# Kernel optimization log

Hardware: AMD Instinct MI355X
Metric: run time of the kernel (lower is better)

Reference implementation:

```python
import jax, jax.numpy as jnp
import numpy as np

EPS = 1e-5

def bn_eval(x, p):
    # p: [4, C] = gamma, beta, running_mean, running_var; channel-last broadcast
    g, b, m, v = p[0], p[1], p[2], p[3]
    return (x - m) * (g / jnp.sqrt(v + EPS)) + b

def _bn_params(k, c):
    k1, k2, k3, k4 = jax.random.split(k, 4)
    gamma = jax.random.uniform(k1, (c,)) + 0.5
    beta = jax.random.normal(k2, (c,)) * 0.1
    mean = jax.random.normal(k3, (c,)) * 0.1
    var = jax.random.uniform(k4, (c,)) + 0.5
    return jnp.stack([gamma, beta, mean, var])

def _lin(k, fan_in, fan_out):
    bound = 1.0 / np.sqrt(fan_in)
    kw, kb = jax.random.split(k)
    w = jax.random.uniform(kw, (fan_in, fan_out), minval=-bound, maxval=bound)
    b = jax.random.uniform(kb, (fan_out,), minval=-bound, maxval=bound)
    return w, b

def setup_inputs() -> dict:
    key = jax.random.key(0)
    B, N, S, C, G = 2, 4096, 16, 256, 8
    ks = jax.random.split(key, 20)
    feats = jax.random.normal(ks[0], (B, N, C), dtype=jnp.float32)
    coords = jax.random.normal(ks[1], (B, N, 3), dtype=jnp.float32)
    index = jax.random.randint(ks[2], (B, N, S), 0, N, dtype=jnp.int32)
    wq, bq = _lin(ks[3], C, C); bnq = _bn_params(ks[4], C)
    wk, bk = _lin(ks[5], C, C); bnk = _bn_params(ks[6], C)
    wv, bv = _lin(ks[7], C, C)
    pm_w1, pm_b1 = _lin(ks[8], 3, C); pm_bn = _bn_params(ks[9], C)
    pm_w2, pm_b2 = _lin(ks[10], C, C)
    pb_w1, pb_b1 = _lin(ks[11], 3, C); pb_bn = _bn_params(ks[12], C)
    pb_w2, pb_b2 = _lin(ks[13], C, C)
    we_w1, we_b1 = _lin(ks[14], C, G); we_bn = _bn_params(ks[15], G)
    we_w2, we_b2 = _lin(ks[16], G, G)
    return dict(feats=feats, coords=coords, index=index,
                wq=wq, bq=bq, bnq=bnq, wk=wk, bk=bk, bnk=bnk, wv=wv, bv=bv,
                pm_w1=pm_w1, pm_b1=pm_b1, pm_bn=pm_bn, pm_w2=pm_w2, pm_b2=pm_b2,
                pb_w1=pb_w1, pb_b1=pb_b1, pb_bn=pb_bn, pb_w2=pb_w2, pb_b2=pb_b2,
                we_w1=we_w1, we_b1=we_b1, we_bn=we_bn, we_w2=we_w2, we_b2=we_b2)

def reference(feats, coords, index,
              wq, bq, bnq, wk, bk, bnk, wv, bv,
              pm_w1, pm_b1, pm_bn, pm_w2, pm_b2,
              pb_w1, pb_b1, pb_bn, pb_w2, pb_b2,
              we_w1, we_b1, we_bn, we_w2, we_b2):
    B, N, C = feats.shape
    S = index.shape[2]
    G = we_w1.shape[1]
    q = jax.nn.relu(bn_eval(feats @ wq + bq, bnq))                       # [B,N,C]
    k = jax.nn.relu(bn_eval(feats @ wk + bk, bnk))                       # [B,N,C]
    v = feats @ wv + bv                                                   # [B,N,C]
    idx = index.reshape(B, N * S)
    key_g = jnp.take_along_axis(k, idx[:, :, None], axis=1).reshape(B, N, S, C)
    val_g = jnp.take_along_axis(v, idx[:, :, None], axis=1).reshape(B, N, S, C)
    crd_g = jnp.take_along_axis(coords, idx[:, :, None], axis=1).reshape(B, N, S, 3)
    relation_qk = key_g - q[:, :, None, :]                                # [B,N,S,C]
    pos = coords[:, :, None, :] - crd_g                                   # [B,N,S,3]
    pem = jax.nn.relu(bn_eval(pos @ pm_w1 + pm_b1, pm_bn)) @ pm_w2 + pm_b2
    relation_qk = relation_qk * pem
    peb = jax.nn.relu(bn_eval(pos @ pb_w1 + pb_b1, pb_bn)) @ pb_w2 + pb_b2
    relation_qk = relation_qk + peb
    val_g = val_g + peb
    w = jax.nn.relu(bn_eval(relation_qk @ we_w1 + we_b1, we_bn)) @ we_w2 + we_b2  # [B,N,S,G]
    w = jax.nn.softmax(w, axis=2)                                         # softmax over neighbors
    val_g = val_g.reshape(B, N, S, G, C // G)
    out = jnp.einsum('bnsgi,bnsg->bngi', val_g, w).reshape(B, N, C)
    return out
```

## Files before the change

kernel.cpp:

```cpp
#include <hip/hip_runtime.h>
#include <hip/hip_bf16.h>


typedef __attribute__((ext_vector_type(8))) short bf16x8_t;
typedef __attribute__((ext_vector_type(4))) float f32x4_t;

#define BN_EPS 1e-5f
#define WSYNC() asm volatile("s_waitcnt lgkmcnt(0)" ::: "memory")

__device__ __forceinline__ float blo(unsigned int v) {
    union { unsigned int u; float f; } x; x.u = v << 16; return x.f;
}
__device__ __forceinline__ float bhi(unsigned int v) {
    union { unsigned int u; float f; } x; x.u = v & 0xffff0000u; return x.f;
}
__device__ __forceinline__ unsigned int fbits(float f) {
    union { float f; unsigned int u; } x; x.f = f; return x.u;
}
__device__ __forceinline__ unsigned short f2b(float f) {
    unsigned int u = fbits(f);
    return (unsigned short)((u + 0x7fffu + ((u >> 16) & 1u)) >> 16);
}
__device__ __forceinline__ float b2f(unsigned short h) {
    union { unsigned int u; float f; } x; x.u = ((unsigned int)h) << 16; return x.f;
}
__device__ __forceinline__ unsigned int f2bpk(float a, float b) {
    union { __hip_bfloat162 h; unsigned int u; } x;
    x.h = __float22bfloat162_rn(make_float2(a, b));
    return x.u;
}
__device__ __forceinline__ unsigned int relpair(unsigned int kb, unsigned int qb,
                                                unsigned int pm_, unsigned int pb_) {
    float r0 = (blo(kb) - blo(qb)) * blo(pm_) + blo(pb_);
    float r1 = (bhi(kb) - bhi(qb)) * bhi(pm_) + bhi(pb_);
    return f2bpk(r0, r1);
}

__global__ __launch_bounds__(256) void k_prep(
    const float* __restrict__ wq, const float* __restrict__ wk,
    const float* __restrict__ wv, const float* __restrict__ pm2,
    const float* __restrict__ pb2,
    const float* __restrict__ pm_w1, const float* __restrict__ pm_b1,
    const float* __restrict__ pm_bn,
    const float* __restrict__ pb_w1, const float* __restrict__ pb_b1,
    const float* __restrict__ pb_bn,
    const float* __restrict__ we_w1,
    const float* __restrict__ bq, const float* __restrict__ bnq,
    const float* __restrict__ bk, const float* __restrict__ bnk,
    const float* __restrict__ bv,
    unsigned short* __restrict__ wsT, unsigned short* __restrict__ w1F,
    unsigned short* __restrict__ we1TF, float* __restrict__ SS)
{
    const int bid = blockIdx.x, t = threadIdx.x;
    if (bid < 160) {
        __shared__ unsigned short T[32][72];
        const int mat = bid >> 5;
        const int kk  = (bid >> 2) & 7;
        const int ntq = bid & 3;
        const float* s = (mat == 0) ? wq : (mat == 1) ? wk : (mat == 2) ? wv
                         : (mat == 3) ? pm2 : pb2;
        {
            int c = t & 63, r0 = t >> 6;
            for (int i = 0; i < 8; ++i) {
                int r = r0 + i * 4;
                T[r][c] = f2b(s[(kk * 32 + r) * 256 + ntq * 64 + c]);
            }
        }
        __syncthreads();
        {
            int seg = t >> 6, lane = t & 63;
            int col = seg * 16 + (lane & 15);
            int kr  = (lane >> 4) * 8;
            unsigned int v[8];
            #pragma unroll
            for (int j = 0; j < 8; ++j) v[j] = T[kr + j][col];
            uint4 o;
            o.x = v[0] | (v[1] << 16);
            o.y = v[2] | (v[3] << 16);
            o.z = v[4] | (v[5] << 16);
            o.w = v[6] | (v[7] << 16);
            *(uint4*)(wsT + mat * 65536 + (ntq * 4 + seg) * 4096 + kk * 512 + lane * 8) = o;
        }
    } else if (bid == 160) {
        int c = t;
        int nt = c >> 4, l15 = c & 15;
        float sm = pm_bn[c] / sqrtf(pm_bn[768 + c] + BN_EPS);
        float sb = pb_bn[c] / sqrtf(pb_bn[768 + c] + BN_EPS);
        float W[2][4];
        W[0][0] = pm_w1[c] * sm; W[0][1] = pm_w1[256 + c] * sm;
        W[0][2] = pm_w1[512 + c] * sm;
        W[0][3] = (pm_b1[c] - pm_bn[512 + c]) * sm + pm_bn[256 + c];
        W[1][0] = pb_w1[c] * sb; W[1][1] = pb_w1[256 + c] * sb;
        W[1][2] = pb_w1[512 + c] * sb;
        W[1][3] = (pb_b1[c] - pb_bn[512 + c]) * sb + pb_bn[256 + c];
        for (int pass = 0; pass < 2; ++pass) {
            unsigned short xh = f2b(W[pass][0]), xl = f2b(W[pass][0] - b2f(xh));
            unsigned short yh = f2b(W[pass][1]), yl = f2b(W[pass][1] - b2f(yh));
            unsigned short zh = f2b(W[pass][2]), zl = f2b(W[pass][2] - b2f(zh));
            unsigned short bh = f2b(W[pass][3]), bl = f2b(W[pass][3] - b2f(bh));
            unsigned short sl[16] = { xh, xh, xl, yh, yh, yl, zh, zh, zl,
                                      bh, bl, 0, 0, 0, 0, 0 };
            for (int q = 0; q < 4; ++q)
                for (int j = 0; j < 8; ++j)
                    w1F[((pass * 16 + nt) * 64 + q * 16 + l15) * 8 + j] =
                        (q < 2) ? sl[q * 8 + j] : (unsigned short)0;
        }
    } else {
        for (int j = 0; j < 8; ++j) {
            int e = t * 8 + j;
            int g = e >> 8, c = e & 255;
            we1TF[g * 256 + c] = f2b(we_w1[c * 8 + g]);
        }
        int c = t;
        float sq = bnq[c] / sqrtf(bnq[768 + c] + BN_EPS);
        SS[c]        = sq;
        SS[256 + c]  = (bq[c] - bnq[512 + c]) * sq + bnq[256 + c];
        float sk = bnk[c] / sqrtf(bnk[768 + c] + BN_EPS);
        SS[512 + c]  = sk;
        SS[768 + c]  = (bk[c] - bnk[512 + c]) * sk + bnk[256 + c];
        SS[1024 + c] = 1.0f;
        SS[1280 + c] = bv[c];
    }
}

__global__ __launch_bounds__(256) void k_qkv(
    const float* __restrict__ feats,
    const unsigned short* __restrict__ wT,
    const float* __restrict__ SS,
    unsigned short* __restrict__ qkv)
{
    __shared__ unsigned short A[32][264];
    const int t    = threadIdx.x;
    const int widx = blockIdx.x >> 8;
    const int mb   = blockIdx.x & 255;

    for (int i = 0; i < 8; ++i) {
        int row = 4 * i + (t >> 6), col = (t & 63) * 4;
        float4 f = *(const float4*)(feats + (mb * 32 + row) * 256 + col);
        *(uint2*)&A[row][col] = make_uint2(f2bpk(f.x, f.y), f2bpk(f.z, f.w));
    }
    __syncthreads();

    const int lane = t & 63, w = t >> 6;
    const int ln15 = lane & 15, quad = lane >> 4;
    const int mt = w & 1, nh = w >> 1;

    bf16x8_t afr[8];
    #pragma unroll
    for (int kk = 0; kk < 8; ++kk)
        afr[kk] = *(const bf16x8_t*)&A[mt * 16 + ln15][kk * 32 + quad * 8];

    const unsigned short* W = wT + widx * 65536;
    unsigned short* dst = qkv + (size_t)widx * 8192 * 256;

    f32x4_t acc[8];
    for (int j = 0; j < 8; ++j) acc[j] = (f32x4_t){0.f, 0.f, 0.f, 0.f};

    #pragma unroll
    for (int kk = 0; kk < 8; ++kk) {
        #pragma unroll
        for (int j = 0; j < 8; ++j) {
            int nt = nh * 8 + j;
            bf16x8_t wfr = *(const bf16x8_t*)(W + ((nt * 8 + kk) * 64 + lane) * 8);
            acc[j] = __builtin_amdgcn_mfma_f32_16x16x32_bf16(wfr, afr[kk], acc[j], 0, 0, 0);
        }
    }

    const float* S = SS + widx * 512;
    const int row = mb * 32 + mt * 16 + ln15;
    #pragma unroll
    for (int j = 0; j < 8; ++j) {
        int n0 = (nh * 8 + j) * 16 + quad * 4;
        float4 s4 = *(const float4*)(S + n0);
        float4 h4 = *(const float4*)(S + 256 + n0);
        float y0 = acc[j][0] * s4.x + h4.x;
        float y1 = acc[j][1] * s4.y + h4.y;
        float y2 = acc[j][2] * s4.z + h4.z;
        float y3 = acc[j][3] * s4.w + h4.w;
        if (widx < 2) {
            y0 = fmaxf(y0, 0.f); y1 = fmaxf(y1, 0.f);
            y2 = fmaxf(y2, 0.f); y3 = fmaxf(y3, 0.f);
        }
        *(uint2*)(dst + (size_t)row * 256 + n0) =
            make_uint2(f2bpk(y0, y1), f2bpk(y2, y3));
    }
}

__global__ __launch_bounds__(512, 4) void k_main(
    const float* __restrict__ coords,
    const int*   __restrict__ index,
    const unsigned short* __restrict__ qm,
    const unsigned short* __restrict__ km,
    const unsigned short* __restrict__ vm,
    const unsigned short* __restrict__ pmw2F,
    const unsigned short* __restrict__ pbw2F,
    const unsigned short* __restrict__ w1F,
    const unsigned short* __restrict__ we1TF,
    const float* __restrict__ pm_b2, const float* __restrict__ pb_b2,
    const float* __restrict__ we_b1, const float* __restrict__ we_bn,
    const float* __restrict__ we_w2, const float* __restrict__ we_b2,
    float* __restrict__ out)
{
    __shared__ unsigned short bufR[64][264];
    __shared__ unsigned short bufP[64][264];
    __shared__ unsigned short posX[64][32];
    __shared__ float us_[8][16][10];
    __shared__ float we2s[8][8];
    __shared__ float web2[8], swe8[8], dwe8[8];

    const int t   = threadIdx.x;
    const int P0  = blockIdx.x * 4;
    const int bb_ = P0 >> 12;
    const int w = t >> 6, lane = t & 63;
    const int ln15 = lane & 15, quad = lane >> 4;
    const int p   = w >> 1, sub = w & 1;
    const int R0  = p * 16;
    const int Pg  = P0 + p;

    const int rg = (bb_ << 12) + index[Pg * 16 + ln15];

    if (t < 64) {
        int m  = t;
        int Pr = P0 + (m >> 4);
        int rs = (bb_ << 12) + index[Pr * 16 + (m & 15)];
        float x = coords[Pr * 3 + 0] - coords[rs * 3 + 0];
        float y = coords[Pr * 3 + 1] - coords[rs * 3 + 1];
        float z = coords[Pr * 3 + 2] - coords[rs * 3 + 2];
        unsigned short xh = f2b(x), xl = f2b(x - b2f(xh));
        unsigned short yh = f2b(y), yl = f2b(y - b2f(yh));
        unsigned short zh = f2b(z), zl = f2b(z - b2f(zh));
        const unsigned short one = 0x3f80;
        posX[m][0] = xh; posX[m][1] = xl; posX[m][2] = xh;
        posX[m][3] = yh; posX[m][4] = yl; posX[m][5] = yh;
        posX[m][6] = zh; posX[m][7] = zl; posX[m][8] = zh;
        posX[m][9] = one; posX[m][10] = one;
        #pragma unroll
        for (int j2 = 11; j2 < 32; ++j2) posX[m][j2] = 0;
        we2s[m >> 3][m & 7] = we_w2[m];
    }
    if (t < 8) {
        float s = we_bn[t] / sqrtf(we_bn[24 + t] + BN_EPS);
        swe8[t] = s;
        dwe8[t] = (we_b1[t] - we_bn[16 + t]) * s + we_bn[8 + t];
        web2[t] = we_b2[t];
    }
    __syncthreads();

    bf16x8_t afrP[4];
    #pragma unroll
    for (int mt = 0; mt < 4; ++mt)
        afrP[mt] = *(const bf16x8_t*)&posX[mt * 16 + ln15][quad * 8];

    {
        f32x4_t hb[2][4];
        for (int ntl = 0; ntl < 2; ++ntl)
            for (int mt = 0; mt < 4; ++mt) hb[ntl][mt] = (f32x4_t){0.f, 0.f, 0.f, 0.f};
        #pragma unroll
        for (int ntl = 0; ntl < 2; ++ntl) {
            int nt = w * 2 + ntl;
            bf16x8_t wfr = *(const bf16x8_t*)(w1F + ((16 + nt) * 64 + lane) * 8);
            #pragma unroll
            for (int mt = 0; mt < 4; ++mt)
                hb[ntl][mt] = __builtin_amdgcn_mfma_f32_16x16x32_bf16(wfr, afrP[mt], hb[ntl][mt], 0, 0, 0);
        }
        #pragma unroll
        for (int ntl = 0; ntl < 2; ++ntl) {
            int cb = w * 32 + ntl * 16 + quad * 4;
            #pragma unroll
            for (int mt = 0; mt < 4; ++mt) {
                unsigned int pk0 = f2bpk(fmaxf(hb[ntl][mt][0], 0.f), fmaxf(hb[ntl][mt][1], 0.f));
                unsigned int pk1 = f2bpk(fmaxf(hb[ntl][mt][2], 0.f), fmaxf(hb[ntl][mt][3], 0.f));
                *(uint2*)&bufR[mt * 16 + ln15][cb] = make_uint2(pk0, pk1);
            }
        }
    }
    __syncthreads();

    f32x4_t accM[2][4];
    for (int ntl = 0; ntl < 2; ++ntl)
        for (int mt = 0; mt < 4; ++mt) accM[ntl][mt] = (f32x4_t){0.f, 0.f, 0.f, 0.f};
    #pragma unroll
    for (int ntl = 0; ntl < 2; ++ntl) {
        int nt = w * 2 + ntl;
        bf16x8_t wfr = *(const bf16x8_t*)(w1F + (nt * 64 + lane) * 8);
        #pragma unroll
        for (int mt = 0; mt < 4; ++mt)
            accM[ntl][mt] = __builtin_amdgcn_mfma_f32_16x16x32_bf16(wfr, afrP[mt], accM[ntl][mt], 0, 0, 0);
    }
    f32x4_t acc[2][4];
    {
        f32x4_t b0 = *(const f32x4_t*)(pb_b2 + (w * 2    ) * 16 + quad * 4);
        f32x4_t b1 = *(const f32x4_t*)(pb_b2 + (w * 2 + 1) * 16 + quad * 4);
        for (int mt = 0; mt < 4; ++mt) { acc[0][mt] = b0; acc[1][mt] = b1; }
    }
    #pragma unroll
    for (int kk = 0; kk < 8; ++kk) {
        bf16x8_t afr[4];
        #pragma unroll
        for (int mt = 0; mt < 4; ++mt)
            afr[mt] = *(const bf16x8_t*)&bufR[mt * 16 + ln15][kk * 32 + quad * 8];
        #pragma unroll
        for (int ntl = 0; ntl < 2; ++ntl) {
            int nt = w * 2 + ntl;
            bf16x8_t wfr = *(const bf16x8_t*)(pbw2F + ((nt * 8 + kk) * 64 + lane) * 8);
            #pragma unroll
            for (int mt = 0; mt < 4; ++mt)
                acc[ntl][mt] = __builtin_amdgcn_mfma_f32_16x16x32_bf16(wfr, afr[mt], acc[ntl][mt], 0, 0, 0);
        }
    }
    #pragma unroll
    for (int ntl = 0; ntl < 2; ++ntl) {
        int cb = w * 32 + ntl * 16 + quad * 4;
        #pragma unroll
        for (int mt = 0; mt < 4; ++mt) {
            unsigned int pk0 = f2bpk(acc[ntl][mt][0], acc[ntl][mt][1]);
            unsigned int pk1 = f2bpk(acc[ntl][mt][2], acc[ntl][mt][3]);
            *(uint2*)&bufP[mt * 16 + ln15][cb] = make_uint2(pk0, pk1);
        }
    }
    __syncthreads();

    #pragma unroll
    for (int ntl = 0; ntl < 2; ++ntl) {
        int cb = w * 32 + ntl * 16 + quad * 4;
        #pragma unroll
        for (int mt = 0; mt < 4; ++mt) {
            unsigned int pk0 = f2bpk(fmaxf(accM[ntl][mt][0], 0.f), fmaxf(accM[ntl][mt][1], 0.f));
            unsigned int pk1 = f2bpk(fmaxf(accM[ntl][mt][2], 0.f), fmaxf(accM[ntl][mt][3], 0.f));
            *(uint2*)&bufR[mt * 16 + ln15][cb] = make_uint2(pk0, pk1);
        }
    }
    __syncthreads();

    uint4 kpre[8];
    #pragma unroll
    for (int kk = 0; kk < 8; ++kk)
        kpre[kk] = *(const uint4*)(km + (size_t)rg * 256 + kk * 32 + quad * 8);
    {
        f32x4_t b0 = *(const f32x4_t*)(pm_b2 + (w * 2    ) * 16 + quad * 4);
        f32x4_t b1 = *(const f32x4_t*)(pm_b2 + (w * 2 + 1) * 16 + quad * 4);
        for (int mt = 0; mt < 4; ++mt) { acc[0][mt] = b0; acc[1][mt] = b1; }
    }
    #pragma unroll
    for (int kk = 0; kk < 8; ++kk) {
        bf16x8_t afr[4];
        #pragma unroll
        for (int mt = 0; mt < 4; ++mt)
            afr[mt] = *(const bf16x8_t*)&bufR[mt * 16 + ln15][kk * 32 + quad * 8];
        #pragma unroll
        for (int ntl = 0; ntl < 2; ++ntl) {
            int nt = w * 2 + ntl;
            bf16x8_t wfr = *(const bf16x8_t*)(pmw2F + ((nt * 8 + kk) * 64 + lane) * 8);
            #pragma unroll
            for (int mt = 0; mt < 4; ++mt)
                acc[ntl][mt] = __builtin_amdgcn_mfma_f32_16x16x32_bf16(wfr, afr[mt], acc[ntl][mt], 0, 0, 0);
        }
    }
    __syncthreads();

    uint4 qpre[8];
    #pragma unroll
    for (int kk = 0; kk < 8; ++kk)
        qpre[kk] = *(const uint4*)(qm + (size_t)Pg * 256 + kk * 32 + quad * 8);
    const int c5 = (sub * 64 + lane) * 2;
    unsigned int vpre[16];
    #pragma unroll
    for (int s = 0; s < 16; ++s) {
        int rv = __shfl(rg, s);
        vpre[s] = *(const unsigned int*)(vm + (size_t)rv * 256 + c5);
    }

    #pragma unroll
    for (int ntl = 0; ntl < 2; ++ntl) {
        int cb = w * 32 + ntl * 16 + quad * 4;
        #pragma unroll
        for (int mt = 0; mt < 4; ++mt) {
            unsigned int pk0 = f2bpk(acc[ntl][mt][0], acc[ntl][mt][1]);
            unsigned int pk1 = f2bpk(acc[ntl][mt][2], acc[ntl][mt][3]);
            *(uint2*)&bufR[mt * 16 + ln15][cb] = make_uint2(pk0, pk1);
        }
    }
    __syncthreads();

    {
        const bf16x8_t bz = {0, 0, 0, 0, 0, 0, 0, 0};
        f32x4_t lacc = {0.f, 0.f, 0.f, 0.f};
        #pragma unroll
        for (int kk = 0; kk < 8; ++kk) {
            int cb8 = kk * 32 + quad * 8;
            uint4 pm4 = *(const uint4*)&bufR[R0 + ln15][cb8];
            uint4 pb4 = *(const uint4*)&bufP[R0 + ln15][cb8];
            uint4 q4  = qpre[kk];
            union { uint4 u; bf16x8_t v; } rr;
            rr.u.x = relpair(kpre[kk].x, q4.x, pm4.x, pb4.x);
            rr.u.y = relpair(kpre[kk].y, q4.y, pm4.y, pb4.y);
            rr.u.z = relpair(kpre[kk].z, q4.z, pm4.z, pb4.z);
            rr.u.w = relpair(kpre[kk].w, q4.w, pm4.w, pb4.w);
            bf16x8_t wfr = bz;
            if (ln15 < 8) wfr = *(const bf16x8_t*)(we1TF + ln15 * 256 + cb8);
            lacc = __builtin_amdgcn_mfma_f32_16x16x32_bf16(wfr, rr.v, lacc, 0, 0, 0);
        }
        if (quad < 2) {
            f32x4_t uv4;
            #pragma unroll
            for (int r = 0; r < 4; ++r) {
                int g = quad * 4 + r;
                uv4[r] = fmaxf(lacc[r] * swe8[g] + dwe8[g], 0.f);
            }
            *(f32x4_t*)&us_[w][ln15][quad * 4] = uv4;
        }
    }
    WSYNC();

    if (lane < 16) {
        int s = lane;
        float uvv[8], l[8];
        #pragma unroll
        for (int g = 0; g < 8; ++g) uvv[g] = us_[w][s][g];
        #pragma unroll
        for (int g = 0; g < 8; ++g) {
            float x = web2[g];
            for (int gp = 0; gp < 8; ++gp) x += uvv[gp] * we2s[gp][g];
            l[g] = x;
        }
        #pragma unroll
        for (int g = 0; g < 8; ++g) us_[w][s][g] = l[g];
    }
    WSYNC();

    if (lane < 8) {
        int g = lane;
        float mx = -1e30f;
        for (int s = 0; s < 16; ++s) mx = fmaxf(mx, us_[w][s][g]);
        float e[16], sum = 0.f;
        for (int s = 0; s < 16; ++s) { e[s] = __expf(us_[w][s][g] - mx); sum += e[s]; }
        float inv = 1.f / sum;
        for (int s = 0; s < 16; ++s) us_[w][s][g] = e[s] * inv;
    }
    WSYNC();

    {
        int g = c5 >> 5;
        float a0 = 0.f, a1 = 0.f;
        #pragma unroll
        for (int s = 0; s < 16; ++s) {
            float wv_ = us_[w][s][g];
            unsigned int v2 = vpre[s];
            unsigned int p2 = *(const unsigned int*)&bufP[R0 + s][c5];
            a0 += wv_ * (blo(v2) + blo(p2));
            a1 += wv_ * (bhi(v2) + bhi(p2));
        }
        *(float2*)(out + (size_t)Pg * 256 + c5) = make_float2(a0, a1);
    }
}

extern "C" void kernel_launch(void* const* d_in, const int* in_sizes, int n_in,
                              void* d_out, int out_size, void* d_ws, size_t ws_size,
                              hipStream_t stream)
{
    const float* feats  = (const float*)d_in[0];
    const float* coords = (const float*)d_in[1];
    const int*   index  = (const int*)d_in[2];
    const float* wq     = (const float*)d_in[3];
    const float* bq     = (const float*)d_in[4];
    const float* bnq    = (const float*)d_in[5];
    const float* wk     = (const float*)d_in[6];
    const float* bk     = (const float*)d_in[7];
    const float* bnk    = (const float*)d_in[8];
    const float* wv     = (const float*)d_in[9];
    const float* bv     = (const float*)d_in[10];
    const float* pm_w1  = (const float*)d_in[11];
    const float* pm_b1  = (const float*)d_in[12];
    const float* pm_bn  = (const float*)d_in[13];
    const float* pm_w2  = (const float*)d_in[14];
    const float* pm_b2  = (const float*)d_in[15];
    const float* pb_w1  = (const float*)d_in[16];
    const float* pb_b1  = (const float*)d_in[17];
    const float* pb_bn  = (const float*)d_in[18];
    const float* pb_w2  = (const float*)d_in[19];
    const float* pb_b2  = (const float*)d_in[20];
    const float* we_w1  = (const float*)d_in[21];
    const float* we_b1  = (const float*)d_in[22];
    const float* we_bn  = (const float*)d_in[23];
    const float* we_w2  = (const float*)d_in[24];
    const float* we_b2  = (const float*)d_in[25];

    unsigned short* qkv   = (unsigned short*)d_ws;
    unsigned short* wsT   = qkv + (size_t)3 * 8192 * 256;
    unsigned short* we1TF = wsT + 5 * 65536;
    unsigned short* w1F   = we1TF + 2048;
    float*          SS    = (float*)(w1F + 16384);

    const size_t need = (size_t)13281280;
    if (ws_size < need) {
        hipMemsetAsync(d_out, 0, (size_t)out_size * 4, stream);
        return;
    }

    k_prep<<<162,  256, 0, stream>>>(wq, wk, wv, pm_w2, pb_w2,
                                     pm_w1, pm_b1, pm_bn,
                                     pb_w1, pb_b1, pb_bn,
                                     we_w1,
                                     bq, bnq, bk, bnk, bv,
                                     wsT, w1F, we1TF, SS);
    k_qkv <<<768,  256, 0, stream>>>(feats, wsT, SS, qkv);
    k_main<<<2048, 512, 0, stream>>>(coords, index,
                                     qkv,
                                     qkv + (size_t)8192 * 256,
                                     qkv + (size_t)2 * 8192 * 256,
                                     wsT + 3 * 65536,
                                     wsT + 4 * 65536,
                                     w1F, we1TF,
                                     pm_b2, pb_b2,
                                     we_b1, we_bn, we_w2, we_b2,
                                     (float*)d_out);
}
```

Measured before the change: 212.4 us.

## Split we1 relation reduction across wave pairs and defer value gather

Previously both waves of a point pair computed the full 256-channel relation/we1 MFMA reduction redundantly. Now each wave handles half the K range and writes partial logits to shared memory, and one wave sums them before the BN, we2 and softmax steps. The k/q prefetch registers are halved, and the value gather is moved after the reduction using neighbor rows cached in shared memory. This adds a block-wide barrier and shared partial buffers, and it lowers register pressure.

```diff
diff --git a/kernel.cpp b/kernel.cpp
--- a/kernel.cpp
+++ b/kernel.cpp
@@ -204,7 +204,9 @@
     __shared__ unsigned short bufR[64][264];
     __shared__ unsigned short bufP[64][264];
     __shared__ unsigned short posX[64][32];
-    __shared__ float us_[8][16][10];
+    __shared__ float usP[2][64][8];
+    __shared__ float us_[64][8];
+    __shared__ int   rowg_[64];
     __shared__ float we2s[8][8];
     __shared__ float web2[8], swe8[8], dwe8[8];
 
@@ -223,6 +225,7 @@
         int m  = t;
         int Pr = P0 + (m >> 4);
         int rs = (bb_ << 12) + index[Pr * 16 + (m & 15)];
+        rowg_[m] = rs;
         float x = coords[Pr * 3 + 0] - coords[rs * 3 + 0];
         float y = coords[Pr * 3 + 1] - coords[rs * 3 + 1];
         float z = coords[Pr * 3 + 2] - coords[rs * 3 + 2];
@@ -332,10 +335,10 @@
     }
     __syncthreads();
 
-    uint4 kpre[8];
-    #pragma unroll
-    for (int kk = 0; kk < 8; ++kk)
-        kpre[kk] = *(const uint4*)(km + (size_t)rg * 256 + kk * 32 + quad * 8);
+    uint4 kpre[4];
+    #pragma unroll
+    for (int kk = 0; kk < 4; ++kk)
+        kpre[kk] = *(const uint4*)(km + (size_t)rg * 256 + (sub * 4 + kk) * 32 + quad * 8);
     {
         f32x4_t b0 = *(const f32x4_t*)(pm_b2 + (w * 2    ) * 16 + quad * 4);
         f32x4_t b1 = *(const f32x4_t*)(pm_b2 + (w * 2 + 1) * 16 + quad * 4);
@@ -358,17 +361,10 @@
     }
     __syncthreads();
 
-    uint4 qpre[8];
-    #pragma unroll
-    for (int kk = 0; kk < 8; ++kk)
-        qpre[kk] = *(const uint4*)(qm + (size_t)Pg * 256 + kk * 32 + quad * 8);
-    const int c5 = (sub * 64 + lane) * 2;
-    unsigned int vpre[16];
-    #pragma unroll
-    for (int s = 0; s < 16; ++s) {
-        int rv = __shfl(rg, s);
-        vpre[s] = *(const unsigned int*)(vm + (size_t)rv * 256 + c5);
-    }
+    uint4 qpre[4];
+    #pragma unroll
+    for (int kk = 0; kk < 4; ++kk)
+        qpre[kk] = *(const uint4*)(qm + (size_t)Pg * 256 + (sub * 4 + kk) * 32 + quad * 8);
 
     #pragma unroll
     for (int ntl = 0; ntl < 2; ++ntl) {
@@ -386,8 +382,8 @@
         const bf16x8_t bz = {0, 0, 0, 0, 0, 0, 0, 0};
         f32x4_t lacc = {0.f, 0.f, 0.f, 0.f};
         #pragma unroll
-        for (int kk = 0; kk < 8; ++kk) {
-            int cb8 = kk * 32 + quad * 8;
+        for (int kk = 0; kk < 4; ++kk) {
+            int cb8 = (sub * 4 + kk) * 32 + quad * 8;
             uint4 pm4 = *(const uint4*)&bufR[R0 + ln15][cb8];
             uint4 pb4 = *(const uint4*)&bufP[R0 + ln15][cb8];
             uint4 q4  = qpre[kk];
@@ -400,51 +396,56 @@
             if (ln15 < 8) wfr = *(const bf16x8_t*)(we1TF + ln15 * 256 + cb8);
             lacc = __builtin_amdgcn_mfma_f32_16x16x32_bf16(wfr, rr.v, lacc, 0, 0, 0);
         }
-        if (quad < 2) {
-            f32x4_t uv4;
-            #pragma unroll
-            for (int r = 0; r < 4; ++r) {
-                int g = quad * 4 + r;
-                uv4[r] = fmaxf(lacc[r] * swe8[g] + dwe8[g], 0.f);
-            }
-            *(f32x4_t*)&us_[w][ln15][quad * 4] = uv4;
-        }
-    }
-    WSYNC();
-
-    if (lane < 16) {
+        if (quad < 2)
+            *(f32x4_t*)&usP[sub][R0 + ln15][quad * 4] = lacc;
+    }
+
+    const int c5 = (sub * 64 + lane) * 2;
+    unsigned int vpre[16];
+    #pragma unroll
+    for (int s = 0; s < 16; ++s) {
+        int rv = rowg_[R0 + s];
+        vpre[s] = *(const unsigned int*)(vm + (size_t)rv * 256 + c5);
+    }
+    __syncthreads();
+
+    if (sub == 0 && lane < 16) {
         int s = lane;
-        float uvv[8], l[8];
-        #pragma unroll
-        for (int g = 0; g < 8; ++g) uvv[g] = us_[w][s][g];
+        float uv[8], l[8];
+        #pragma unroll
+        for (int g = 0; g < 8; ++g) {
+            float x = usP[0][R0 + s][g] + usP[1][R0 + s][g];
+            uv[g] = fmaxf(x * swe8[g] + dwe8[g], 0.f);
+        }
         #pragma unroll
         for (int g = 0; g < 8; ++g) {
             float x = web2[g];
-            for (int gp = 0; gp < 8; ++gp) x += uvv[gp] * we2s[gp][g];
+            #pragma unroll
+            for (int gp = 0; gp < 8; ++gp) x += uv[gp] * we2s[gp][g];
             l[g] = x;
         }
         #pragma unroll
-        for (int g = 0; g < 8; ++g) us_[w][s][g] = l[g];
+        for (int g = 0; g < 8; ++g) us_[R0 + s][g] = l[g];
     }
     WSYNC();
 
-    if (lane < 8) {
+    if (sub == 0 && lane < 8) {
         int g = lane;
         float mx = -1e30f;
-        for (int s = 0; s < 16; ++s) mx = fmaxf(mx, us_[w][s][g]);
+        for (int s = 0; s < 16; ++s) mx = fmaxf(mx, us_[R0 + s][g]);
         float e[16], sum = 0.f;
-        for (int s = 0; s < 16; ++s) { e[s] = __expf(us_[w][s][g] - mx); sum += e[s]; }
+        for (int s = 0; s < 16; ++s) { e[s] = __expf(us_[R0 + s][g] - mx); sum += e[s]; }
         float inv = 1.f / sum;
-        for (int s = 0; s < 16; ++s) us_[w][s][g] = e[s] * inv;
-    }
-    WSYNC();
+        for (int s = 0; s < 16; ++s) us_[R0 + s][g] = e[s] * inv;
+    }
+    __syncthreads();
 
     {
         int g = c5 >> 5;
         float a0 = 0.f, a1 = 0.f;
         #pragma unroll
         for (int s = 0; s < 16; ++s) {
-            float wv_ = us_[w][s][g];
+            float wv_ = us_[R0 + s][g];
             unsigned int v2 = vpre[s];
             unsigned int p2 = *(const unsigned int*)&bufP[R0 + s][c5];
             a0 += wv_ * (blo(v2) + blo(p2));
```

After: 185.9 us. 1.14x faster.
